# Performance work log

Hardware: AMD Instinct MI355X
Metric: run time of the kernel (lower is better)

## Reference

```python
import jax, jax.numpy as jnp
import numpy as np
import math

C = 512          # channels
K = 3            # conv kernel size
DILATIONS = (1, 3, 5)
RATIO = 2        # up/down sample ratio
FK = 12          # FIR anti-alias kernel size


def kaiser_sinc_filter1d(cutoff, half_width, kernel_size):
    # BigVGAN alias-free kaiser-windowed sinc lowpass filter
    half_size = kernel_size // 2
    delta_f = 4.0 * half_width
    A = 2.285 * (half_size - 1) * math.pi * delta_f + 7.95
    if A > 50.0:
        beta = 0.1102 * (A - 8.7)
    elif A >= 21.0:
        beta = 0.5842 * (A - 21.0) ** 0.4 + 0.07886 * (A - 21.0)
    else:
        beta = 0.0
    window = np.kaiser(kernel_size, beta)
    if kernel_size % 2 == 0:
        time = np.arange(-half_size, half_size) + 0.5
    else:
        time = np.arange(kernel_size) - half_size
    filt = 2.0 * cutoff * window * np.sinc(2.0 * cutoff * time)
    filt = filt / filt.sum()
    return jnp.asarray(filt, dtype=jnp.float32)

# Up/Down both use cutoff=0.5/ratio, half_width=0.6/ratio, kernel=12
AA_FILTER = kaiser_sinc_filter1d(0.5 / RATIO, 0.6 / RATIO, FK)

UP_PAD = FK // RATIO - 1                               # 5 (replicate pad before transpose conv)
UP_PAD_LEFT = UP_PAD * RATIO + (FK - RATIO) // 2       # 15
UP_PAD_RIGHT = UP_PAD * RATIO + (FK - RATIO + 1) // 2  # 15
DN_PAD_LEFT = FK // 2 - 1                              # 5 (even kernel)
DN_PAD_RIGHT = FK // 2                                 # 6


def _depthwise_conv(x, filt, stride=1, lhs_dilation=1, padding=(0, 0)):
    c = x.shape[1]
    w = jnp.broadcast_to(filt.reshape(1, 1, -1), (c, 1, filt.shape[0]))
    return jax.lax.conv_general_dilated(
        x, w, window_strides=(stride,), padding=[padding],
        lhs_dilation=(lhs_dilation,), dimension_numbers=('NCH', 'OIH', 'NCH'),
        feature_group_count=c)


def upsample2x(x):
    # replicate pad, depthwise transposed conv (lhs-dilated conv w/ flipped kernel), crop, scale
    x = jnp.pad(x, ((0, 0), (0, 0), (UP_PAD, UP_PAD)), mode='edge')
    y = RATIO * _depthwise_conv(x, AA_FILTER[::-1], lhs_dilation=RATIO,
                                padding=(FK - 1, FK - 1))
    return y[..., UP_PAD_LEFT:-UP_PAD_RIGHT]


def downsample2x(x):
    x = jnp.pad(x, ((0, 0), (0, 0), (DN_PAD_LEFT, DN_PAD_RIGHT)), mode='edge')
    return _depthwise_conv(x, AA_FILTER, stride=RATIO)


def snake_log(x, alpha, beta):
    # use_log_scale=True: alpha/beta are exponentiated; x + 1/(b+1e-5) * sin(a*x)^2
    a = jnp.exp(alpha)[None, :, None]
    b = jnp.exp(beta)[None, :, None]
    return x + (1.0 / (b + 1e-5)) * jnp.square(jnp.sin(x * a))


def aliasing_activation(x, alpha, beta):
    return downsample2x(snake_log(upsample2x(x), alpha, beta))


def weight_norm_conv1d(x, v, g, bias, dilation):
    # torch weight_norm dim=0: W[o] = g[o] * v[o] / ||v[o]||
    norm = jnp.sqrt(jnp.sum(v * v, axis=(1, 2), keepdims=True))
    w = g[:, None, None] * v / norm
    pad = (K * dilation - dilation) // 2
    y = jax.lax.conv_general_dilated(
        x, w, window_strides=(1,), padding=[(pad, pad)],
        rhs_dilation=(dilation,), dimension_numbers=('NCH', 'OIH', 'NCH'))
    return y + bias[None, :, None]


def setup_inputs() -> dict:
    key = jax.random.key(0)
    ks = jax.random.split(key, 12)
    B, T = 16, 4096
    return {
        'x': jax.random.normal(ks[0], (B, C, T), dtype=jnp.float32),
        'float_masks': jnp.ones((B, 1, T), dtype=jnp.float32),
        'in_snake_alpha': 0.1 * jax.random.normal(ks[1], (3, C), dtype=jnp.float32),
        'in_snake_beta': 0.1 * jax.random.normal(ks[2], (3, C), dtype=jnp.float32),
        'out_snake_alpha': 0.1 * jax.random.normal(ks[3], (3, C), dtype=jnp.float32),
        'out_snake_beta': 0.1 * jax.random.normal(ks[4], (3, C), dtype=jnp.float32),
        'in_conv_v': 0.05 * jax.random.normal(ks[5], (3, C, C, K), dtype=jnp.float32),
        'in_conv_g': 1.0 + 0.01 * jax.random.normal(ks[6], (3, C), dtype=jnp.float32),
        'in_conv_b': 0.01 * jax.random.normal(ks[7], (3, C), dtype=jnp.float32),
        'out_conv_v': 0.05 * jax.random.normal(ks[8], (3, C, C, K), dtype=jnp.float32),
        'out_conv_g': 1.0 + 0.01 * jax.random.normal(ks[9], (3, C), dtype=jnp.float32),
        'out_conv_b': 0.01 * jax.random.normal(ks[10], (3, C), dtype=jnp.float32),
    }


def reference(x, float_masks, in_snake_alpha, in_snake_beta, out_snake_alpha,
              out_snake_beta, in_conv_v, in_conv_g, in_conv_b, out_conv_v,
              out_conv_g, out_conv_b):
    for i, dilation in enumerate(DILATIONS):
        residuals = x
        x = aliasing_activation(x, in_snake_alpha[i], in_snake_beta[i]) * float_masks
        x = weight_norm_conv1d(x, in_conv_v[i], in_conv_g[i], in_conv_b[i], dilation)
        x = aliasing_activation(x, out_snake_alpha[i], out_snake_beta[i]) * float_masks
        x = weight_norm_conv1d(x, out_conv_v[i], out_conv_g[i], out_conv_b[i], 1)
        x = x + residuals
    return x * float_masks
```

## Files before the change

kernel.cpp:

```cpp
#include <hip/hip_runtime.h>
#include <cmath>

#define BN_ 16
#define CN_ 512
#define TN_ 4096
#define TPAD_ 4112
#define PADR_ 8

typedef float f32x4 __attribute__((ext_vector_type(4)));
typedef __bf16 bf16x8 __attribute__((ext_vector_type(8)));
typedef unsigned short u16x8 __attribute__((ext_vector_type(8)));

struct AAFilt { float g0[6]; float g1[6]; float fE[6]; float fO[6]; };

__device__ __forceinline__ unsigned short f2bf(float f) {
  unsigned u = __builtin_bit_cast(unsigned, f);
  u = (u + 0x7fffu + ((u >> 16) & 1u)) >> 16;
  return (unsigned short)u;
}
__device__ __forceinline__ float bf2f(unsigned short h) {
  return __builtin_bit_cast(float, (unsigned)h << 16);
}
__device__ __forceinline__ float to_f(float x) { return x; }
__device__ __forceinline__ float to_f(unsigned short x) { return bf2f(x); }

__device__ __forceinline__ void gld16(const void* g, void* l) {
  __builtin_amdgcn_global_load_lds((const __attribute__((address_space(1))) void*)g,
                                   (__attribute__((address_space(3))) void*)l,
                                   16, 0, 0);
}

__global__ __launch_bounds__(256) void prep_w(
    const float* __restrict__ vin, const float* __restrict__ gin,
    const float* __restrict__ vout, const float* __restrict__ gout,
    unsigned short* __restrict__ wpack)
{
  const int o = blockIdx.x;
  const int l = blockIdx.y;
  const int i = l >> 1, oc = l & 1;
  const float* v = (oc ? vout : vin) + (size_t)i * CN_ * CN_ * 3 + (size_t)o * CN_ * 3;
  const float g = (oc ? gout : gin)[i * CN_ + o];
  const int tid = threadIdx.x;

  float a = 0.f;
  for (int j = tid; j < 1536; j += 256) { float x = v[j]; a += x * x; }
  #pragma unroll
  for (int off = 32; off > 0; off >>= 1) a += __shfl_down(a, off);
  __shared__ float red[4];
  if ((tid & 63) == 0) red[tid >> 6] = a;
  __syncthreads();
  const float tot = red[0] + red[1] + red[2] + red[3];
  const float scale = g / sqrtf(tot);
  unsigned short* wl = wpack + (size_t)l * 3 * CN_ * CN_;
  for (int j = tid; j < 1536; j += 256) {
    int c = j / 3, k = j - 3 * c;
    wl[((size_t)k * CN_ + o) * CN_ + c] = f2bf(v[j] * scale);
  }
}

__global__ __launch_bounds__(256) void transpose_in(
    const float* __restrict__ src, float* __restrict__ dst)
{
  __shared__ float tile[32][33];
  const int b = blockIdx.z, c0 = blockIdx.y * 32, t0 = blockIdx.x * 32;
  const int tx = threadIdx.x & 31, ty = threadIdx.x >> 5;
  const float* s = src + ((size_t)b * CN_ + c0) * TN_ + t0;
  #pragma unroll
  for (int j = 0; j < 32; j += 8) tile[ty + j][tx] = s[(size_t)(ty + j) * TN_ + tx];
  __syncthreads();
  float* d = dst + ((size_t)b * TN_ + t0) * CN_ + c0;
  #pragma unroll
  for (int j = 0; j < 32; j += 8) d[(size_t)(ty + j) * CN_ + tx] = tile[tx][ty + j];
}

template <typename TIN>
__global__ __launch_bounds__(512) void act_kernel(
    const TIN* __restrict__ src, unsigned short* __restrict__ dst,
    const float* __restrict__ alpha, const float* __restrict__ beta,
    const float* __restrict__ mask, AAFilt F)
{
  const int c = threadIdx.x;
  const int b = blockIdx.y;
  const int seg = blockIdx.x;
  const int t0 = seg << 7;
  const float av = expf(alpha[c]);
  const float ib = 1.0f / (expf(beta[c]) + 1e-5f);
  const TIN* row = src + (size_t)b * TN_ * CN_ + c;
  unsigned short* drow = dst + (size_t)b * TPAD_ * CN_ + c;
  const float* mrow = mask + (size_t)b * TN_;

  if (seg == 0)  { for (int p = 0; p < PADR_; ++p) drow[(size_t)p * CN_] = 0; }
  if (seg == 31) { for (int p = 0; p < PADR_; ++p) drow[(size_t)(TPAD_ - PADR_ + p) * CN_] = 0; }

  auto ldx = [&](int t) -> float {
    t = t < 0 ? 0 : (t > TN_ - 1 ? TN_ - 1 : t);
    return to_f(row[(size_t)t * CN_]);
  };

  float xw[6];
  #pragma unroll
  for (int j = 0; j < 6; ++j) xw[j] = ldx(t0 - 5 + j);
  float sE[6], sO[6];
  #pragma unroll
  for (int j = 0; j < 6; ++j) { sE[j] = 0.f; sO[j] = 0.f; }
  float s_last = 0.f;

  auto step = [&](int tau, bool emit) {
    float uO = 0.f, uE = 0.f;
    #pragma unroll
    for (int j = 0; j < 6; ++j) { uO += F.g1[j] * xw[j]; uE += F.g0[j] * xw[j]; }
    float so = __sinf(uO * av); float sOn = uO + ib * so * so;
    float se = __sinf(uE * av); float sEn = uE + ib * se * se;
    if (tau + 2 == TN_ - 1) s_last = sOn;
    if (tau + 2 >= TN_) sOn = s_last;
    if (tau + 3 >= TN_) sEn = s_last;
    #pragma unroll
    for (int j = 0; j < 5; ++j) { sE[j] = sE[j + 1]; sO[j] = sO[j + 1]; }
    sE[5] = sEn; sO[5] = sOn;
    if (emit) {
      float d = 0.f;
      #pragma unroll
      for (int j = 0; j < 6; ++j) d += F.fE[j] * sE[j] + F.fO[j] * sO[j];
      d *= mrow[tau];
      drow[(size_t)(PADR_ + tau) * CN_] = f2bf(d);
    }
    #pragma unroll
    for (int j = 0; j < 5; ++j) xw[j] = xw[j + 1];
    xw[5] = ldx(tau + 6);
  };

  for (int w = 0; w < 5; ++w) step(t0 - 5 + w, false);
  if (t0 == 0) {
    float s0 = sE[3];
    sE[1] = s0; sE[2] = s0;
    sO[1] = s0; sO[2] = s0; sO[3] = s0;
  }
  for (int t = t0; t < t0 + 128; ++t) step(t, true);
}

#define ASZ (272 * 32)

template <int MODE, int DIL>
__global__ __launch_bounds__(256, 2) void conv_kernel(
    const unsigned short* __restrict__ act,
    const unsigned short* __restrict__ wp,
    const float* __restrict__ bias,
    const float* __restrict__ res,
    const float* __restrict__ mask,
    void* __restrict__ outp)
{
  __shared__ __align__(16) unsigned short lA[2 * ASZ];

  const int tid = threadIdx.x;
  const int bid = blockIdx.x;
  const int xcd = bid & 7, j = bid >> 3;
  const int ob = j & 3, tile = j >> 2;
  const int tt = tile * 8 + xcd;
  const int b = tt >> 4;
  const int t0 = (tt & 15) << 8;
  const int o0 = ob << 7;

  const int lane = tid & 63;
  const int wave = tid >> 6;
  const int wm = wave >> 1, wn = wave & 1;
  const int l15 = lane & 15, q4 = lane >> 4;
  const int q8 = q4 * 8;

  const f32x4 zero = {0.f, 0.f, 0.f, 0.f};
  f32x4 acc[8][4];
  #pragma unroll
  for (int a = 0; a < 8; ++a)
    #pragma unroll
    for (int n = 0; n < 4; ++n) acc[a][n] = zero;

  const unsigned short* aBase = act + ((size_t)b * TPAD_ + t0) * CN_;
  const int ob0 = o0 + wn * 64 + l15;

  auto stageA = [&](int bufi, int cb) {
    const int c0 = cb * 32;
    unsigned short* Ad = lA + (size_t)bufi * ASZ;
    #pragma unroll
    for (int it = 0; it < 4; ++it) {
      int p = tid + it * 256;
      int r = p >> 2, pq = p & 3, gq = pq ^ ((r >> 1) & 3);
      gld16(aBase + (size_t)r * CN_ + c0 + gq * 8, Ad + (size_t)p * 8);
    }
    if (tid < 64) {
      int p = tid + 1024;
      int r = p >> 2, pq = p & 3, gq = pq ^ ((r >> 1) & 3);
      gld16(aBase + (size_t)r * CN_ + c0 + gq * 8, Ad + (size_t)p * 8);
    }
  };

  stageA(0, 0);
  __syncthreads();

  for (int cb = 0; cb < 16; ++cb) {
    const unsigned short* A = lA + (size_t)(cb & 1) * ASZ;
    if (cb < 15) stageA((cb & 1) ^ 1, cb + 1);
    const int c0 = cb * 32;

    #pragma unroll
    for (int k = 0; k < 3; ++k) {
      bf16x8 bfr[4];
      #pragma unroll
      for (int ni = 0; ni < 4; ++ni) {
        const unsigned short* bp =
            wp + ((size_t)(k * CN_ + ob0 + ni * 16)) * CN_ + c0 + q8;
        bfr[ni] = __builtin_bit_cast(bf16x8, *reinterpret_cast<const u16x8*>(bp));
      }
      bf16x8 af[8];
      const int rb0 = wm * 128 + l15 + PADR_ + (k - 1) * DIL;
      #pragma unroll
      for (int mi = 0; mi < 8; ++mi) {
        int r = rb0 + mi * 16;
        int q = q4 ^ ((r >> 1) & 3);
        af[mi] = __builtin_bit_cast(bf16x8,
                   *reinterpret_cast<const u16x8*>(A + ((size_t)r * 4 + q) * 8));
      }
      #pragma unroll
      for (int mi = 0; mi < 8; ++mi)
        #pragma unroll
        for (int ni = 0; ni < 4; ++ni)
          acc[mi][ni] = __builtin_amdgcn_mfma_f32_16x16x32_bf16(
              af[mi], bfr[ni], acc[mi][ni], 0, 0, 0);
    }
    if (cb < 15) __syncthreads();
  }

  const int obase = ob0;
  const int tbase = t0 + wm * 128 + q4 * 4;

  if (MODE == 0) {
    unsigned short* O = (unsigned short*)outp + (size_t)b * TN_ * CN_;
    #pragma unroll
    for (int ni = 0; ni < 4; ++ni) {
      float bv = bias[obase + ni * 16];
      #pragma unroll
      for (int mi = 0; mi < 8; ++mi) {
        #pragma unroll
        for (int r = 0; r < 4; ++r) {
          int t = tbase + mi * 16 + r;
          O[(size_t)t * CN_ + obase + ni * 16] = f2bf(acc[mi][ni][r] + bv);
        }
      }
    }
  } else if (MODE == 1) {
    float* O = (float*)outp + (size_t)b * TN_ * CN_;
    const float* R = res + (size_t)b * TN_ * CN_;
    #pragma unroll
    for (int ni = 0; ni < 4; ++ni) {
      float bv = bias[obase + ni * 16];
      #pragma unroll
      for (int mi = 0; mi < 8; ++mi) {
        #pragma unroll
        for (int r = 0; r < 4; ++r) {
          int t = tbase + mi * 16 + r;
          size_t ix = (size_t)t * CN_ + obase + ni * 16;
          O[ix] = acc[mi][ni][r] + bv + R[ix];
        }
      }
    }
  } else {
    float* O = (float*)outp + (size_t)b * CN_ * TN_;
    const float* R = res + (size_t)b * TN_ * CN_;
    const float* M = mask + (size_t)b * TN_;
    float bv[4];
    #pragma unroll
    for (int ni = 0; ni < 4; ++ni) bv[ni] = bias[obase + ni * 16];
    #pragma unroll
    for (int mi = 0; mi < 8; ++mi) {
      int t = tbase + mi * 16;
      f32x4 mv = *reinterpret_cast<const f32x4*>(M + t);
      #pragma unroll
      for (int ni = 0; ni < 4; ++ni) {
        f32x4 v;
        #pragma unroll
        for (int r = 0; r < 4; ++r)
          v[r] = (acc[mi][ni][r] + bv[ni] + R[(size_t)(t + r) * CN_ + obase + ni * 16]) * mv[r];
        *reinterpret_cast<f32x4*>(O + (size_t)(obase + ni * 16) * TN_ + t) = v;
      }
    }
  }
}

static double bi0(double x) {
  double s = 1.0, t = 1.0, q = x * x * 0.25;
  for (int k = 1; k < 50; ++k) { t *= q / ((double)k * (double)k); s += t; if (t < 1e-18 * s) break; }
  return s;
}
static void make_filt(AAFilt* F) {
  const double PI = 3.14159265358979323846;
  double A = 2.285 * 5.0 * PI * 1.2 + 7.95;
  double beta;
  if (A > 50.0) beta = 0.1102 * (A - 8.7);
  else if (A >= 21.0) beta = 0.5842 * pow(A - 21.0, 0.4) + 0.07886 * (A - 21.0);
  else beta = 0.0;
  double i0b = bi0(beta);
  double f[12], sum = 0.0;
  for (int n = 0; n < 12; ++n) {
    double xx = 2.0 * n / 11.0 - 1.0;
    double w = bi0(beta * sqrt(fmax(0.0, 1.0 - xx * xx))) / i0b;
    double tt = (double)(n - 6) + 0.5;
    double arg = 0.5 * tt;
    double snc = sin(PI * arg) / (PI * arg);
    f[n] = 0.5 * w * snc;
    sum += f[n];
  }
  for (int n = 0; n < 12; ++n) f[n] /= sum;
  for (int j = 0; j < 6; ++j) {
    F->g0[j] = (float)(2.0 * f[11 - 2 * j]);
    F->g1[j] = (float)(2.0 * f[10 - 2 * j]);
    F->fE[j] = (float)f[2 * j + 1];
    F->fO[j] = (float)f[2 * j];
  }
}

extern "C" void kernel_launch(void* const* d_in, const int* in_sizes, int n_in,
                              void* d_out, int out_size, void* d_ws, size_t ws_size,
                              hipStream_t stream)
{
  (void)in_sizes; (void)n_in; (void)out_size; (void)ws_size;
  const float* x    = (const float*)d_in[0];
  const float* mask = (const float*)d_in[1];
  const float* inA  = (const float*)d_in[2];
  const float* inB  = (const float*)d_in[3];
  const float* outA = (const float*)d_in[4];
  const float* outB = (const float*)d_in[5];
  const float* vin  = (const float*)d_in[6];
  const float* gin  = (const float*)d_in[7];
  const float* bin  = (const float*)d_in[8];
  const float* vout = (const float*)d_in[9];
  const float* gout = (const float*)d_in[10];
  const float* bout = (const float*)d_in[11];

  char* ws = (char*)d_ws;
  float* xta           = (float*)ws;
  unsigned short* actb = (unsigned short*)(ws + 134217728);
  unsigned short* y1   = (unsigned short*)(ws + 134217728 + 67371008);
  unsigned short* wpk  = (unsigned short*)(ws + 134217728 + 67371008 + 67108864);

  AAFilt F; make_filt(&F);

  prep_w<<<dim3(512, 6), dim3(256), 0, stream>>>(vin, gin, vout, gout, wpk);
  transpose_in<<<dim3(128, 16, 16), dim3(256), 0, stream>>>(x, xta);

  float* dof = (float*)d_out;

  act_kernel<float><<<dim3(32, 16), dim3(512), 0, stream>>>(
      xta, actb, inA + 0 * CN_, inB + 0 * CN_, mask, F);
  conv_kernel<0, 1><<<dim3(1024), dim3(256), 0, stream>>>(
      actb, wpk + (size_t)0 * 3 * CN_ * CN_, bin + 0 * CN_, nullptr, mask, (void*)y1);
  act_kernel<unsigned short><<<dim3(32, 16), dim3(512), 0, stream>>>(
      y1, actb, outA + 0 * CN_, outB + 0 * CN_, mask, F);
  conv_kernel<1, 1><<<dim3(1024), dim3(256), 0, stream>>>(
      actb, wpk + (size_t)1 * 3 * CN_ * CN_, bout + 0 * CN_, xta, mask, (void*)dof);

  act_kernel<float><<<dim3(32, 16), dim3(512), 0, stream>>>(
      dof, actb, inA + 1 * CN_, inB + 1 * CN_, mask, F);
  conv_kernel<0, 3><<<dim3(1024), dim3(256), 0, stream>>>(
      actb, wpk + (size_t)2 * 3 * CN_ * CN_, bin + 1 * CN_, nullptr, mask, (void*)y1);
  act_kernel<unsigned short><<<dim3(32, 16), dim3(512), 0, stream>>>(
      y1, actb, outA + 1 * CN_, outB + 1 * CN_, mask, F);
  conv_kernel<1, 1><<<dim3(1024), dim3(256), 0, stream>>>(
      actb, wpk + (size_t)3 * 3 * CN_ * CN_, bout + 1 * CN_, dof, mask, (void*)xta);

  act_kernel<float><<<dim3(32, 16), dim3(512), 0, stream>>>(
      xta, actb, inA + 2 * CN_, inB + 2 * CN_, mask, F);
  conv_kernel<0, 5><<<dim3(1024), dim3(256), 0, stream>>>(
      actb, wpk + (size_t)4 * 3 * CN_ * CN_, bin + 2 * CN_, nullptr, mask, (void*)y1);
  act_kernel<unsigned short><<<dim3(32, 16), dim3(512), 0, stream>>>(
      y1, actb, outA + 2 * CN_, outB + 2 * CN_, mask, F);
  conv_kernel<2, 1><<<dim3(1024), dim3(256), 0, stream>>>(
      actb, wpk + (size_t)5 * 3 * CN_ * CN_, bout + 2 * CN_, xta, mask, d_out);
}
```

Measured before the change: 1.307 ms.

## Restructure conv kernel to 1024-thread blocks covering all outputs with LDS-staged weights

Each conv block now computes 128 time steps for all 512 output channels with 16 waves, instead of 256 time steps by 128 channels. The weight tile for each 32-channel slice is staged into LDS and shared by all waves, replacing direct per-wave global loads of weights. Activation tiles are read once per block rather than once per output-channel block. The trade-offs are a larger LDS footprint of roughly 114 KB per block, which limits occupancy, and a weight stage that is not double-buffered, so each K-step waits on two extra barriers. The launch_bounds hint of 4 blocks per CU cannot be met with that LDS size.

```diff
diff --git a/kernel.cpp b/kernel.cpp
--- a/kernel.cpp
+++ b/kernel.cpp
@@ -138,10 +138,12 @@
   for (int t = t0; t < t0 + 128; ++t) step(t, true);
 }
 
-#define ASZ (272 * 32)
+#define AROWS 144
+#define ASZ (AROWS * 32)
+#define BSZ (3 * 512 * 32)
 
 template <int MODE, int DIL>
-__global__ __launch_bounds__(256, 2) void conv_kernel(
+__global__ __launch_bounds__(1024, 4) void conv_kernel(
     const unsigned short* __restrict__ act,
     const unsigned short* __restrict__ wp,
     const float* __restrict__ bias,
@@ -150,86 +152,91 @@
     void* __restrict__ outp)
 {
   __shared__ __align__(16) unsigned short lA[2 * ASZ];
+  __shared__ __align__(16) unsigned short lB[BSZ];
 
   const int tid = threadIdx.x;
   const int bid = blockIdx.x;
-  const int xcd = bid & 7, j = bid >> 3;
-  const int ob = j & 3, tile = j >> 2;
-  const int tt = tile * 8 + xcd;
-  const int b = tt >> 4;
-  const int t0 = (tt & 15) << 8;
-  const int o0 = ob << 7;
+  const int b = bid >> 5;
+  const int t0 = (bid & 31) << 7;
 
   const int lane = tid & 63;
   const int wave = tid >> 6;
-  const int wm = wave >> 1, wn = wave & 1;
+  const int wm = wave >> 3, wn = wave & 7;
   const int l15 = lane & 15, q4 = lane >> 4;
-  const int q8 = q4 * 8;
 
   const f32x4 zero = {0.f, 0.f, 0.f, 0.f};
-  f32x4 acc[8][4];
-  #pragma unroll
-  for (int a = 0; a < 8; ++a)
+  f32x4 acc[4][4];
+  #pragma unroll
+  for (int a = 0; a < 4; ++a)
     #pragma unroll
     for (int n = 0; n < 4; ++n) acc[a][n] = zero;
 
   const unsigned short* aBase = act + ((size_t)b * TPAD_ + t0) * CN_;
-  const int ob0 = o0 + wn * 64 + l15;
 
   auto stageA = [&](int bufi, int cb) {
-    const int c0 = cb * 32;
-    unsigned short* Ad = lA + (size_t)bufi * ASZ;
-    #pragma unroll
-    for (int it = 0; it < 4; ++it) {
-      int p = tid + it * 256;
+    if (tid < 576) {
+      const int c0 = cb * 32;
+      unsigned short* Ad = lA + (size_t)bufi * ASZ;
+      int p = tid;
       int r = p >> 2, pq = p & 3, gq = pq ^ ((r >> 1) & 3);
       gld16(aBase + (size_t)r * CN_ + c0 + gq * 8, Ad + (size_t)p * 8);
     }
-    if (tid < 64) {
-      int p = tid + 1024;
-      int r = p >> 2, pq = p & 3, gq = pq ^ ((r >> 1) & 3);
-      gld16(aBase + (size_t)r * CN_ + c0 + gq * 8, Ad + (size_t)p * 8);
-    }
   };
+  auto stageB = [&](int cb) {
+    const int c0 = cb * 32;
+    #pragma unroll
+    for (int it = 0; it < 6; ++it) {
+      int p = tid + it * 1024;
+      int k = p >> 11, rem = p & 2047, ol = rem >> 2, pq = rem & 3;
+      int gq = pq ^ ((ol >> 1) & 3);
+      gld16(wp + ((size_t)(k * CN_) + ol) * CN_ + c0 + gq * 8,
+            lB + (size_t)p * 8);
+    }
+  };
 
   stageA(0, 0);
+  stageB(0);
   __syncthreads();
 
   for (int cb = 0; cb < 16; ++cb) {
     const unsigned short* A = lA + (size_t)(cb & 1) * ASZ;
     if (cb < 15) stageA((cb & 1) ^ 1, cb + 1);
-    const int c0 = cb * 32;
 
     #pragma unroll
     for (int k = 0; k < 3; ++k) {
-      bf16x8 bfr[4];
-      #pragma unroll
-      for (int ni = 0; ni < 4; ++ni) {
-        const unsigned short* bp =
-            wp + ((size_t)(k * CN_ + ob0 + ni * 16)) * CN_ + c0 + q8;
-        bfr[ni] = __builtin_bit_cast(bf16x8, *reinterpret_cast<const u16x8*>(bp));
-      }
-      bf16x8 af[8];
-      const int rb0 = wm * 128 + l15 + PADR_ + (k - 1) * DIL;
-      #pragma unroll
-      for (int mi = 0; mi < 8; ++mi) {
+      bf16x8 af[4], bfr[4];
+      const int rb0 = 8 + wm * 64 + l15 + (k - 1) * DIL;
+      #pragma unroll
+      for (int mi = 0; mi < 4; ++mi) {
         int r = rb0 + mi * 16;
         int q = q4 ^ ((r >> 1) & 3);
         af[mi] = __builtin_bit_cast(bf16x8,
                    *reinterpret_cast<const u16x8*>(A + ((size_t)r * 4 + q) * 8));
       }
       #pragma unroll
-      for (int mi = 0; mi < 8; ++mi)
+      for (int ni = 0; ni < 4; ++ni) {
+        int ol = wn * 64 + ni * 16 + l15;
+        int q = q4 ^ ((ol >> 1) & 3);
+        bfr[ni] = __builtin_bit_cast(bf16x8,
+                    *reinterpret_cast<const u16x8*>(lB + (((size_t)k * CN_ + ol) * 4 + q) * 8));
+      }
+      #pragma unroll
+      for (int mi = 0; mi < 4; ++mi)
         #pragma unroll
         for (int ni = 0; ni < 4; ++ni)
           acc[mi][ni] = __builtin_amdgcn_mfma_f32_16x16x32_bf16(
               af[mi], bfr[ni], acc[mi][ni], 0, 0, 0);
     }
-    if (cb < 15) __syncthreads();
-  }
-
-  const int obase = ob0;
-  const int tbase = t0 + wm * 128 + q4 * 4;
+
+    if (cb < 15) {
+      __syncthreads();
+      stageB(cb + 1);
+      __syncthreads();
+    }
+  }
+
+  const int obase = wn * 64 + l15;
+  const int tbase = t0 + wm * 64 + q4 * 4;
 
   if (MODE == 0) {
     unsigned short* O = (unsigned short*)outp + (size_t)b * TN_ * CN_;
@@ -237,7 +244,7 @@
     for (int ni = 0; ni < 4; ++ni) {
       float bv = bias[obase + ni * 16];
       #pragma unroll
-      for (int mi = 0; mi < 8; ++mi) {
+      for (int mi = 0; mi < 4; ++mi) {
         #pragma unroll
         for (int r = 0; r < 4; ++r) {
           int t = tbase + mi * 16 + r;
@@ -252,7 +259,7 @@
     for (int ni = 0; ni < 4; ++ni) {
       float bv = bias[obase + ni * 16];
       #pragma unroll
-      for (int mi = 0; mi < 8; ++mi) {
+      for (int mi = 0; mi < 4; ++mi) {
         #pragma unroll
         for (int r = 0; r < 4; ++r) {
           int t = tbase + mi * 16 + r;
@@ -269,7 +276,7 @@
     #pragma unroll
     for (int ni = 0; ni < 4; ++ni) bv[ni] = bias[obase + ni * 16];
     #pragma unroll
-    for (int mi = 0; mi < 8; ++mi) {
+    for (int mi = 0; mi < 4; ++mi) {
       int t = tbase + mi * 16;
       f32x4 mv = *reinterpret_cast<const f32x4*>(M + t);
       #pragma unroll
@@ -349,28 +356,28 @@
 
   act_kernel<float><<<dim3(32, 16), dim3(512), 0, stream>>>(
       xta, actb, inA + 0 * CN_, inB + 0 * CN_, mask, F);
-  conv_kernel<0, 1><<<dim3(1024), dim3(256), 0, stream>>>(
+  conv_kernel<0, 1><<<dim3(512), dim3(1024), 0, stream>>>(
       actb, wpk + (size_t)0 * 3 * CN_ * CN_, bin + 0 * CN_, nullptr, mask, (void*)y1);
   act_kernel<unsigned short><<<dim3(32, 16), dim3(512), 0, stream>>>(
       y1, actb, outA + 0 * CN_, outB + 0 * CN_, mask, F);
-  conv_kernel<1, 1><<<dim3(1024), dim3(256), 0, stream>>>(
+  conv_kernel<1, 1><<<dim3(512), dim3(1024), 0, stream>>>(
       actb, wpk + (size_t)1 * 3 * CN_ * CN_, bout + 0 * CN_, xta, mask, (void*)dof);
 
   act_kernel<float><<<dim3(32, 16), dim3(512), 0, stream>>>(
       dof, actb, inA + 1 * CN_, inB + 1 * CN_, mask, F);
-  conv_kernel<0, 3><<<dim3(1024), dim3(256), 0, stream>>>(
+  conv_kernel<0, 3><<<dim3(512), dim3(1024), 0, stream>>>(
       actb, wpk + (size_t)2 * 3 * CN_ * CN_, bin + 1 * CN_, nullptr, mask, (void*)y1);
   act_kernel<unsigned short><<<dim3(32, 16), dim3(512), 0, stream>>>(
       y1, actb, outA + 1 * CN_, outB + 1 * CN_, mask, F);
-  conv_kernel<1, 1><<<dim3(1024), dim3(256), 0, stream>>>(
+  conv_kernel<1, 1><<<dim3(512), dim3(1024), 0, stream>>>(
       actb, wpk + (size_t)3 * 3 * CN_ * CN_, bout + 1 * CN_, dof, mask, (void*)xta);
 
   act_kernel<float><<<dim3(32, 16), dim3(512), 0, stream>>>(
       xta, actb, inA + 2 * CN_, inB + 2 * CN_, mask, F);
-  conv_kernel<0, 5><<<dim3(1024), dim3(256), 0, stream>>>(
+  conv_kernel<0, 5><<<dim3(512), dim3(1024), 0, stream>>>(
       actb, wpk + (size_t)4 * 3 * CN_ * CN_, bin + 2 * CN_, nullptr, mask, (void*)y1);
   act_kernel<unsigned short><<<dim3(32, 16), dim3(512), 0, stream>>>(
       y1, actb, outA + 2 * CN_, outB + 2 * CN_, mask, F);
-  conv_kernel<2, 1><<<dim3(1024), dim3(256), 0, stream>>>(
+  conv_kernel<2, 1><<<dim3(512), dim3(1024), 0, stream>>>(
       actb, wpk + (size_t)5 * 3 * CN_ * CN_, bout + 2 * CN_, xta, mask, d_out);
 }
```

After: 1.474 ms. +12.8%, slower.
